# Kernel optimization log

Measured on AMD Instinct MI355X. Metric: run time of the kernel, lower is better.

Reference implementation:

```python
import jax, jax.numpy as jnp
import numpy as np

BEV_H = 128; BEV_W = 128; HEADS = 8; POINTS = 4; NUM_LAYERS = 6
PC = (-51.2, -51.2, -5.0, 51.2, 51.2, 3.0)
EPS = 1e-5


def _layernorm(x, g, b):
    m = x.mean(-1, keepdims=True)
    v = x.var(-1, keepdims=True)
    return (x - m) * jax.lax.rsqrt(v + 1e-5) * g + b


def _bilinear(feat, loc):
    # feat: (H, W, D); loc: (..., 2) normalized xy in [0, 1]; zero padding outside.
    H, W = feat.shape[0], feat.shape[1]
    ix = loc[..., 0] * W - 0.5
    iy = loc[..., 1] * H - 0.5
    x0 = jnp.floor(ix); y0 = jnp.floor(iy)
    fx = ix - x0; fy = iy - y0
    out = 0.0
    for dx in (0, 1):
        for dy in (0, 1):
            xi = x0 + dx; yi = y0 + dy
            w = (fx if dx else 1.0 - fx) * (fy if dy else 1.0 - fy)
            m = (xi >= 0) & (xi < W) & (yi >= 0) & (yi < H)
            xi_c = jnp.clip(xi, 0, W - 1).astype(jnp.int32)
            yi_c = jnp.clip(yi, 0, H - 1).astype(jnp.int32)
            out = out + (w * m)[..., None] * feat[yi_c, xi_c]
    return out


def _deform_grid(q, value, H, W, ref, ow, ob, aw, ab):
    # Deformable attention over a (H, W) grid of values; q: (Nq, C), value: (H*W, C).
    Nq, C = q.shape
    hd = C // HEADS
    v = value.reshape(H, W, HEADS, hd).transpose(2, 0, 1, 3)            # (h, H, W, hd)
    off = (q @ ow + ob).reshape(Nq, HEADS, POINTS, 2)
    loc = ref[:, None, None, :] + off / jnp.array([W, H], q.dtype)      # (Nq, h, P, 2)
    attn = jax.nn.softmax((q @ aw + ab).reshape(Nq, HEADS, POINTS), axis=-1)
    sampled = jax.vmap(_bilinear)(v, loc.transpose(1, 0, 2, 3))         # (h, Nq, P, hd)
    return jnp.einsum('hnpd,nhp->nhd', sampled, attn).reshape(Nq, C)


def _sca(q, feats, ref_cam, valid, ow, ob, aw, ab):
    # Spatial cross-attention: feats (Ncam, h, Hf, Wf, hd), ref_cam (Ncam, Nq, P, 2),
    # valid (Ncam, Nq, P) float mask of in-frustum projections.
    Nq, C = q.shape
    Hf, Wf = feats.shape[2], feats.shape[3]
    off = (q @ ow + ob).reshape(Nq, HEADS, POINTS, 2)
    loc = ref_cam[:, None] + (off / jnp.array([Wf, Hf], q.dtype)).transpose(1, 0, 2, 3)[None]
    # loc: (Ncam, h, Nq, P, 2)
    attn = jax.nn.softmax((q @ aw + ab).reshape(Nq, HEADS, POINTS), axis=-1)
    sampled = jax.vmap(jax.vmap(_bilinear))(feats, loc)                 # (Ncam, h, Nq, P, hd)
    num = jnp.einsum('chnpd,nhp,cnp->nhd', sampled, attn, valid)
    cnt = jnp.maximum(valid.sum((0, 2)), 1.0)                           # (Nq,)
    return (num / cnt[:, None, None]).reshape(Nq, C)


def _forward(image_feats, camera_intrinsics, camera_extrinsics, prev_bev, bev_embed,
             tsa_vw, tsa_vb, tsa_ow, tsa_ob, tsa_aw, tsa_ab, tsa_pw, tsa_pb,
             sca_vw, sca_vb, sca_ow, sca_ob, sca_aw, sca_ab, sca_pw, sca_pb,
             ffn_w1, ffn_b1, ffn_w2, ffn_b2,
             ln1_g, ln1_b, ln2_g, ln2_b, ln3_g, ln3_b):
    Ncam, C, Hf, Wf = image_feats.shape
    hd = C // HEADS
    Nq = BEV_H * BEV_W
    dt = image_feats.dtype
    feats_flat = image_feats.transpose(0, 2, 3, 1).reshape(Ncam * Hf * Wf, C)

    # 2D reference points for temporal self-attention (each query's own cell).
    xs = (jnp.arange(BEV_W, dtype=dt) + 0.5) / BEV_W
    ys = (jnp.arange(BEV_H, dtype=dt) + 0.5) / BEV_H
    gx, gy = jnp.meshgrid(xs, ys)                                       # (H, W) each
    ref2d = jnp.stack([gx.reshape(-1), gy.reshape(-1)], -1)             # (Nq, 2)

    # 3D pillar reference points projected into each camera.
    xm = PC[0] + gx.reshape(-1) * (PC[3] - PC[0])
    ym = PC[1] + gy.reshape(-1) * (PC[4] - PC[1])
    zm = PC[2] + (jnp.arange(POINTS, dtype=dt) + 0.5) / POINTS * (PC[5] - PC[2])
    ref3d = jnp.stack([
        jnp.broadcast_to(xm[:, None], (Nq, POINTS)),
        jnp.broadcast_to(ym[:, None], (Nq, POINTS)),
        jnp.broadcast_to(zm[None, :], (Nq, POINTS)),
        jnp.ones((Nq, POINTS), dt)], -1)                                # (Nq, P, 4)
    ego2cam = jnp.linalg.inv(camera_extrinsics[0])                      # (Ncam, 4, 4)
    pcam = jnp.einsum('cij,npj->cnpi', ego2cam, ref3d)[..., :3]
    img = jnp.einsum('cij,cnpj->cnpi', camera_intrinsics[0], pcam)
    z = img[..., 2]
    un = img[..., 0] / (jnp.maximum(z, EPS) * Wf)
    vn = img[..., 1] / (jnp.maximum(z, EPS) * Hf)
    valid = ((z > EPS) & (un >= 0) & (un <= 1) & (vn >= 0) & (vn <= 1)).astype(dt)
    ref_cam = jnp.stack([un, vn], -1)                                   # (Ncam, Nq, P, 2)

    q = bev_embed                                                       # (Nq, C)
    prev = prev_bev[:, 0, :]                                            # (Nq, C), B = 1
    for l in range(NUM_LAYERS):
        # Temporal self-attention: deformable sampling from prev BEV + current BEV.
        v_prev = prev @ tsa_vw[l] + tsa_vb[l]
        v_cur = q @ tsa_vw[l] + tsa_vb[l]
        a = 0.5 * (_deform_grid(q, v_prev, BEV_H, BEV_W, ref2d, tsa_ow[l], tsa_ob[l], tsa_aw[l], tsa_ab[l])
                   + _deform_grid(q, v_cur, BEV_H, BEV_W, ref2d, tsa_ow[l], tsa_ob[l], tsa_aw[l], tsa_ab[l]))
        q = _layernorm(q + a @ tsa_pw[l] + tsa_pb[l], ln1_g[l], ln1_b[l])
        # Spatial cross-attention over multi-camera image features.
        v_img = (feats_flat @ sca_vw[l] + sca_vb[l]).reshape(Ncam, Hf, Wf, HEADS, hd).transpose(0, 3, 1, 2, 4)
        a = _sca(q, v_img, ref_cam, valid, sca_ow[l], sca_ob[l], sca_aw[l], sca_ab[l])
        q = _layernorm(q + a @ sca_pw[l] + sca_pb[l], ln2_g[l], ln2_b[l])
        # FFN
        a = jax.nn.relu(q @ ffn_w1[l] + ffn_b1[l]) @ ffn_w2[l] + ffn_b2[l]
        q = _layernorm(q + a, ln3_g[l], ln3_b[l])
    return q.T.reshape(1, C, BEV_H, BEV_W)


def setup_inputs() -> dict:
    key = jax.random.key(0)
    ks = iter(jax.random.split(key, 80))
    def nrm(shape, s=0.02):
        return jax.random.normal(next(ks), shape, jnp.float32) * s
    C, L, Ncam, Hf, Wf = 256, NUM_LAYERS, 6, 58, 100
    Nq = BEV_H * BEV_W
    HP, HP2 = HEADS * POINTS, HEADS * POINTS * 2
    # Structured nuScenes-like cameras: 6 yaws at 60 deg, intrinsics at feature-map scale.
    extr = np.zeros((1, Ncam, 4, 4), np.float32)
    for c in range(Ncam):
        t = c * np.pi / 3.0
        f = np.array([np.cos(t), np.sin(t), 0.0])
        xc = np.array([np.sin(t), -np.cos(t), 0.0])
        yc = np.array([0.0, 0.0, -1.0])
        extr[0, c, :3, :3] = np.stack([xc, yc, f], axis=1)
        extr[0, c, :3, 3] = 1.5 * f + np.array([0.0, 0.0, 1.5])
        extr[0, c, 3, 3] = 1.0
    intr = np.zeros((1, Ncam, 3, 3), np.float32)
    intr[0, :, 0, 0] = 80.0; intr[0, :, 1, 1] = 80.0
    intr[0, :, 0, 2] = Wf / 2.0; intr[0, :, 1, 2] = Hf / 2.0
    intr[0, :, 2, 2] = 1.0
    return {
        'image_feats': jax.random.normal(next(ks), (Ncam, C, Hf, Wf), jnp.float32),
        'camera_intrinsics': jnp.asarray(intr),
        'camera_extrinsics': jnp.asarray(extr),
        'prev_bev': jax.random.normal(next(ks), (Nq, 1, C), jnp.float32),
        'bev_embed': nrm((Nq, C)),
        'tsa_vw': nrm((L, C, C)), 'tsa_vb': jnp.zeros((L, C), jnp.float32),
        'tsa_ow': nrm((L, C, HP2)), 'tsa_ob': nrm((L, HP2), 2.0),
        'tsa_aw': nrm((L, C, HP)), 'tsa_ab': jnp.zeros((L, HP), jnp.float32),
        'tsa_pw': nrm((L, C, C)), 'tsa_pb': jnp.zeros((L, C), jnp.float32),
        'sca_vw': nrm((L, C, C)), 'sca_vb': jnp.zeros((L, C), jnp.float32),
        'sca_ow': nrm((L, C, HP2)), 'sca_ob': nrm((L, HP2), 2.0),
        'sca_aw': nrm((L, C, HP)), 'sca_ab': jnp.zeros((L, HP), jnp.float32),
        'sca_pw': nrm((L, C, C)), 'sca_pb': jnp.zeros((L, C), jnp.float32),
        'ffn_w1': nrm((L, C, 2 * C)), 'ffn_b1': jnp.zeros((L, 2 * C), jnp.float32),
        'ffn_w2': nrm((L, 2 * C, C)), 'ffn_b2': jnp.zeros((L, C), jnp.float32),
        'ln1_g': jnp.ones((L, C), jnp.float32), 'ln1_b': jnp.zeros((L, C), jnp.float32),
        'ln2_g': jnp.ones((L, C), jnp.float32), 'ln2_b': jnp.zeros((L, C), jnp.float32),
        'ln3_g': jnp.ones((L, C), jnp.float32), 'ln3_b': jnp.zeros((L, C), jnp.float32),
    }


def reference(image_feats, camera_intrinsics, camera_extrinsics, prev_bev, bev_embed,
              tsa_vw, tsa_vb, tsa_ow, tsa_ob, tsa_aw, tsa_ab, tsa_pw, tsa_pb,
              sca_vw, sca_vb, sca_ow, sca_ob, sca_aw, sca_ab, sca_pw, sca_pb,
              ffn_w1, ffn_b1, ffn_w2, ffn_b2,
              ln1_g, ln1_b, ln2_g, ln2_b, ln3_g, ln3_b):
    return _forward(image_feats, camera_intrinsics, camera_extrinsics, prev_bev, bev_embed,
                    tsa_vw, tsa_vb, tsa_ow, tsa_ob, tsa_aw, tsa_ab, tsa_pw, tsa_pb,
                    sca_vw, sca_vb, sca_ow, sca_ob, sca_aw, sca_ab, sca_pw, sca_pb,
                    ffn_w1, ffn_b1, ffn_w2, ffn_b2,
                    ln1_g, ln1_b, ln2_g, ln2_b, ln3_g, ln3_b)
```

## Files before the change

kernel.cpp:

```cpp
#include <hip/hip_runtime.h>
#include <hip/hip_bf16.h>
#include <math.h>

typedef __hip_bfloat16 bf16;

#define NQ      16384
#define CDIM    256
#define NHEADS  8
#define NPOINTS 4
#define NCAM    6
#define HF      58
#define WF      100
#define HWF     (HF*WF)
#define NFEAT   (NCAM*HWF)
#define HD      32
#define NLAYERS 6

typedef __attribute__((ext_vector_type(8))) short short8;
typedef __attribute__((ext_vector_type(4))) float floatx4;

__device__ __forceinline__ float toF(float x) { return x; }
__device__ __forceinline__ float toF(bf16 x) { return __bfloat162float(x); }
__device__ __forceinline__ void storeD(float* p, float v) { *p = v; }
__device__ __forceinline__ void storeD(bf16* p, float v) { *p = __float2bfloat16(v); }

__device__ __forceinline__ float bfLo(unsigned u) { return __uint_as_float(u << 16); }
__device__ __forceinline__ float bfHi(unsigned u) { return __uint_as_float(u & 0xffff0000u); }

__device__ __forceinline__ void gload_lds16(const bf16* g, bf16* l) {
    __builtin_amdgcn_global_load_lds(
        (const __attribute__((address_space(1))) void*)(g),
        (__attribute__((address_space(3))) void*)(l), 16, 0, 0);
}

template <typename DT, bool RELU, bool STAGE>
__global__ __launch_bounds__(256) void gemm_mfma(
    const bf16* __restrict__ A, const bf16* __restrict__ BT,
    const float* __restrict__ bias, DT* __restrict__ D,
    int M, int N, int K, size_t sB, size_t sBias, size_t sD)
{
    int z = blockIdx.z;
    BT += (size_t)z * sB;
    bias += (size_t)z * sBias;
    D += (size_t)z * sD;

    __shared__ bf16 smem[STAGE ? 128 * 136 : 128 * 64];
    bf16* As = smem;
    bf16* Bs = smem + 128 * 32;

    int tid = threadIdx.x;
    int lane = tid & 63, w = tid >> 6;
    int wm = w & 1, wn = w >> 1;
    int l15 = lane & 15, quad = lane >> 4;
    int bm = blockIdx.y * 128, bn = blockIdx.x * 128;

    floatx4 acc[4][4];
#pragma unroll
    for (int i = 0; i < 4; i++)
#pragma unroll
        for (int j = 0; j < 4; j++)
            acc[i][j] = (floatx4){0.f, 0.f, 0.f, 0.f};

    int rsub = lane >> 2;
    int kc   = (lane & 3) * 8;

    for (int k0 = 0; k0 < K; k0 += 32) {
#pragma unroll
        for (int h = 0; h < 2; h++) {
            int r0 = w * 32 + h * 16;
            int gm = bm + r0 + rsub;
            if (gm > M - 1) gm = M - 1;
            gload_lds16(A + (size_t)gm * K + k0 + kc, &As[r0 * 32]);
            gload_lds16(BT + (size_t)(bn + r0 + rsub) * K + k0 + kc, &Bs[r0 * 32]);
        }
        __syncthreads();

        short8 a[4], b[4];
#pragma unroll
        for (int i = 0; i < 4; i++)
            a[i] = *(const short8*)(&As[(wm * 64 + i * 16 + l15) * 32 + quad * 8]);
#pragma unroll
        for (int j = 0; j < 4; j++)
            b[j] = *(const short8*)(&Bs[(wn * 64 + j * 16 + l15) * 32 + quad * 8]);
#pragma unroll
        for (int i = 0; i < 4; i++)
#pragma unroll
            for (int j = 0; j < 4; j++)
                acc[i][j] = __builtin_amdgcn_mfma_f32_16x16x32_bf16(
                    a[i], b[j], acc[i][j], 0, 0, 0);
        __syncthreads();
    }

    if (STAGE) {
#pragma unroll
        for (int i = 0; i < 4; i++) {
#pragma unroll
            for (int j = 0; j < 4; j++) {
                int col = wn * 64 + j * 16 + l15;
                float bv = bias[bn + col];
#pragma unroll
                for (int r = 0; r < 4; r++) {
                    int row = wm * 64 + i * 16 + quad * 4 + r;
                    float v = acc[i][j][r] + bv;
                    if (RELU) v = fmaxf(v, 0.f);
                    smem[row * 136 + col] = __float2bfloat16(v);
                }
            }
        }
        __syncthreads();
        int lr0 = tid >> 4;
        int ck  = tid & 15;
#pragma unroll
        for (int pass = 0; pass < 8; pass++) {
            int lr = pass * 16 + lr0;
            int gm = bm + lr;
            if (gm < M) {
                uint4 v = *(const uint4*)(&smem[lr * 136 + ck * 8]);
                *(uint4*)((bf16*)D + (size_t)gm * N + bn + ck * 8) = v;
            }
        }
    } else {
#pragma unroll
        for (int i = 0; i < 4; i++) {
#pragma unroll
            for (int j = 0; j < 4; j++) {
                int col = bn + wn * 64 + j * 16 + l15;
                float bv = bias[col];
#pragma unroll
                for (int r = 0; r < 4; r++) {
                    int row = bm + wm * 64 + i * 16 + quad * 4 + r;
                    if (row < M) {
                        float v = acc[i][j][r] + bv;
                        if (RELU) v = fmaxf(v, 0.f);
                        storeD(&D[(size_t)row * N + col], v);
                    }
                }
            }
        }
    }
}

__global__ __launch_bounds__(256) void gemm_tsa(
    const bf16* __restrict__ A, const bf16* __restrict__ BT,
    const float* __restrict__ bias,
    bf16* __restrict__ vgrid, float* __restrict__ offlog)
{
    int bn3 = blockIdx.x;
    int bm = blockIdx.y * 128;
    if (bn3 == 2 && bm < NQ) return;
    int bn = bn3 * 128;

    __shared__ bf16 As[128 * 32];
    __shared__ bf16 Bs[128 * 32];

    int tid = threadIdx.x;
    int lane = tid & 63, w = tid >> 6;
    int wm = w & 1, wn = w >> 1;
    int l15 = lane & 15, quad = lane >> 4;

    floatx4 acc[4][4];
#pragma unroll
    for (int i = 0; i < 4; i++)
#pragma unroll
        for (int j = 0; j < 4; j++)
            acc[i][j] = (floatx4){0.f, 0.f, 0.f, 0.f};

    int rsub = lane >> 2;
    int kc   = (lane & 3) * 8;

    for (int k0 = 0; k0 < 256; k0 += 32) {
#pragma unroll
        for (int h = 0; h < 2; h++) {
            int r0 = w * 32 + h * 16;
            gload_lds16(A + (size_t)(bm + r0 + rsub) * 256 + k0 + kc, &As[r0 * 32]);
            gload_lds16(BT + (size_t)(bn + r0 + rsub) * 256 + k0 + kc, &Bs[r0 * 32]);
        }
        __syncthreads();

        short8 a[4], b[4];
#pragma unroll
        for (int i = 0; i < 4; i++)
            a[i] = *(const short8*)(&As[(wm * 64 + i * 16 + l15) * 32 + quad * 8]);
#pragma unroll
        for (int j = 0; j < 4; j++)
            b[j] = *(const short8*)(&Bs[(wn * 64 + j * 16 + l15) * 32 + quad * 8]);
#pragma unroll
        for (int i = 0; i < 4; i++)
#pragma unroll
            for (int j = 0; j < 4; j++)
                acc[i][j] = __builtin_amdgcn_mfma_f32_16x16x32_bf16(
                    a[i], b[j], acc[i][j], 0, 0, 0);
        __syncthreads();
    }

#pragma unroll
    for (int i = 0; i < 4; i++) {
#pragma unroll
        for (int j = 0; j < 4; j++) {
            int col = bn + wn * 64 + j * 16 + l15;
            float bv = bias[col];
#pragma unroll
            for (int r = 0; r < 4; r++) {
                int row = bm + wm * 64 + i * 16 + quad * 4 + r;
                float v = acc[i][j][r] + bv;
                if (bn3 < 2) {
                    int n = row & (NQ - 1);
                    int cur = row >= NQ;
                    size_t idx = ((size_t)n * 64 + (col >> 2)) * 8 + cur * 4 + (col & 3);
                    vgrid[idx] = __float2bfloat16(v);
                } else {
                    offlog[(size_t)(row - NQ) * 128 + (col - 256)] = v;
                }
            }
        }
    }
}

__global__ __launch_bounds__(512) void gemm_ln(
    const bf16* __restrict__ A, const bf16* __restrict__ BT,
    const float* __restrict__ bias,
    bf16* __restrict__ qb,
    const float* __restrict__ g, const float* __restrict__ b,
    int K)
{
    __shared__ bf16 As[64 * 32];
    __shared__ bf16 Bs[256 * 32];
    __shared__ float red[2][64][4];
    __shared__ float stats[2][64];

    int tid = threadIdx.x;
    int lane = tid & 63, w = tid >> 6;
    int wm = w & 1, wn = w >> 1;
    int l15 = lane & 15, quad = lane >> 4;
    int bm = blockIdx.x * 64;

    floatx4 acc[2][4];
#pragma unroll
    for (int i = 0; i < 2; i++)
#pragma unroll
        for (int j = 0; j < 4; j++)
            acc[i][j] = (floatx4){0.f, 0.f, 0.f, 0.f};

    int rsub = lane >> 2;
    int kc   = (lane & 3) * 8;

    for (int k0 = 0; k0 < K; k0 += 32) {
#pragma unroll
        for (int h = 0; h < 2; h++) {
            int r0 = w * 32 + h * 16;
            gload_lds16(BT + (size_t)(r0 + rsub) * K + k0 + kc, &Bs[r0 * 32]);
        }
        if (w < 4)
            gload_lds16(A + (size_t)(bm + w * 16 + rsub) * K + k0 + kc,
                        &As[w * 16 * 32]);
        __syncthreads();

        short8 a[2], bfr[4];
#pragma unroll
        for (int i = 0; i < 2; i++)
            a[i] = *(const short8*)(&As[(wm * 32 + i * 16 + l15) * 32 + quad * 8]);
#pragma unroll
        for (int j = 0; j < 4; j++)
            bfr[j] = *(const short8*)(&Bs[(wn * 64 + j * 16 + l15) * 32 + quad * 8]);
#pragma unroll
        for (int i = 0; i < 2; i++)
#pragma unroll
            for (int j = 0; j < 4; j++)
                acc[i][j] = __builtin_amdgcn_mfma_f32_16x16x32_bf16(
                    a[i], bfr[j], acc[i][j], 0, 0, 0);
        __syncthreads();
    }

    float x[2][4][4];
#pragma unroll
    for (int i = 0; i < 2; i++) {
#pragma unroll
        for (int j = 0; j < 4; j++) {
            int col = wn * 64 + j * 16 + l15;
            float bv = bias[col];
#pragma unroll
            for (int r = 0; r < 4; r++) {
                int row = bm + wm * 32 + i * 16 + quad * 4 + r;
                x[i][j][r] = toF(qb[(size_t)row * CDIM + col]) + acc[i][j][r] + bv;
            }
        }
    }
#pragma unroll
    for (int i = 0; i < 2; i++) {
#pragma unroll
        for (int r = 0; r < 4; r++) {
            float s = x[i][0][r] + x[i][1][r] + x[i][2][r] + x[i][3][r];
            float sq = x[i][0][r] * x[i][0][r] + x[i][1][r] * x[i][1][r] +
                       x[i][2][r] * x[i][2][r] + x[i][3][r] * x[i][3][r];
#pragma unroll
            for (int m = 1; m < 16; m <<= 1) {
                s += __shfl_xor(s, m);
                sq += __shfl_xor(sq, m);
            }
            if (l15 == 0) {
                int rl = wm * 32 + i * 16 + quad * 4 + r;
                red[0][rl][wn] = s;
                red[1][rl][wn] = sq;
            }
        }
    }
    __syncthreads();
    if (tid < 64) {
        float s = red[0][tid][0] + red[0][tid][1] + red[0][tid][2] + red[0][tid][3];
        float sq = red[1][tid][0] + red[1][tid][1] + red[1][tid][2] + red[1][tid][3];
        float mean = s * (1.f / CDIM);
        float var = fmaxf(sq * (1.f / CDIM) - mean * mean, 0.f);
        stats[0][tid] = mean;
        stats[1][tid] = rsqrtf(var + 1e-5f);
    }
    __syncthreads();
#pragma unroll
    for (int i = 0; i < 2; i++) {
#pragma unroll
        for (int j = 0; j < 4; j++) {
            int col = wn * 64 + j * 16 + l15;
            float gc = g[col], bc = b[col];
#pragma unroll
            for (int r = 0; r < 4; r++) {
                int rl = wm * 32 + i * 16 + quad * 4 + r;
                int row = bm + rl;
                float y = (x[i][j][r] - stats[0][rl]) * stats[1][rl] * gc + bc;
                qb[(size_t)row * CDIM + col] = __float2bfloat16(y);
            }
        }
    }
}

__global__ void wt_cvt_kernel(const float* __restrict__ W, bf16* __restrict__ WT,
                              int K, int N)
{
    __shared__ float tile[32][33];
    int l = blockIdx.z;
    const float* Wl = W + (size_t)l * K * N;
    bf16* WTl = WT + (size_t)l * K * N;
    int k0 = blockIdx.x * 32, n0 = blockIdx.y * 32;
    int tx = threadIdx.x, ty = threadIdx.y;
    for (int i = 0; i < 32; i += 8)
        tile[ty + i][tx] = Wl[(size_t)(k0 + ty + i) * N + n0 + tx];
    __syncthreads();
    for (int i = 0; i < 32; i += 8)
        WTl[(size_t)(n0 + ty + i) * K + k0 + tx] = __float2bfloat16(tile[tx][ty + i]);
}

__global__ void pack_tsa_kernel(const float* __restrict__ vw, const float* __restrict__ vb,
                                const float* __restrict__ ow, const float* __restrict__ ob,
                                const float* __restrict__ aw, const float* __restrict__ ab,
                                bf16* __restrict__ WT, float* __restrict__ BIAS)
{
    int n = blockIdx.x;
    int l = blockIdx.y;
    int k = threadIdx.x;
    float v = 0.f;
    if (n < 256)      v = vw[((size_t)l * 256 + k) * 256 + n];
    else if (n < 320) v = ow[((size_t)l * 256 + k) * 64 + (n - 256)];
    else if (n < 352) v = aw[((size_t)l * 256 + k) * 32 + (n - 320)];
    WT[((size_t)l * 384 + n) * 256 + k] = __float2bfloat16(v);
    if (k == 0) {
        float bv = 0.f;
        if (n < 256)      bv = vb[l * 256 + n];
        else if (n < 320) bv = ob[l * 64 + (n - 256)];
        else if (n < 352) bv = ab[l * 32 + (n - 320)];
        BIAS[l * 384 + n] = bv;
    }
}

__global__ void pack_offattn_kernel(const float* __restrict__ ow, const float* __restrict__ ob,
                                    const float* __restrict__ aw, const float* __restrict__ ab,
                                    bf16* __restrict__ WT, float* __restrict__ BIAS)
{
    int l = blockIdx.y;
    int n = blockIdx.x;
    int k = threadIdx.x;
    float v = 0.f;
    if (n < 64)      v = ow[((size_t)l * 256 + k) * 64 + n];
    else if (n < 96) v = aw[((size_t)l * 256 + k) * 32 + (n - 64)];
    WT[((size_t)l * 128 + n) * 256 + k] = __float2bfloat16(v);
    if (k == 0) {
        float bv = 0.f;
        if (n < 64)      bv = ob[l * 64 + n];
        else if (n < 96) bv = ab[l * 32 + (n - 64)];
        BIAS[l * 128 + n] = bv;
    }
}

__global__ void feats_cvt_kernel(const float* __restrict__ in, bf16* __restrict__ outT)
{
    __shared__ float tile[32][33];
    int c = blockIdx.z;
    int r0 = blockIdx.x * 32, ch0 = blockIdx.y * 32;
    int tx = threadIdx.x, ty = threadIdx.y;
    for (int i = 0; i < 32; i += 8) {
        int r = r0 + tx, ch = ch0 + ty + i;
        tile[ty + i][tx] = (r < HWF) ? in[((size_t)c * CDIM + ch) * HWF + r] : 0.f;
    }
    __syncthreads();
    for (int i = 0; i < 32; i += 8) {
        int r = r0 + ty + i, ch = ch0 + tx;
        if (r < HWF)
            outT[((size_t)c * HWF + r) * CDIM + ch] = __float2bfloat16(tile[tx][ty + i]);
    }
}

__global__ __launch_bounds__(256) void cvt_bf16_kernel(const float* __restrict__ in,
                                                       bf16* __restrict__ out, int n)
{
    int i = blockIdx.x * 256 + threadIdx.x;
    if (i < n) out[i] = __float2bfloat16(in[i]);
}

__global__ void invert4_kernel(const float* __restrict__ extr, float* __restrict__ ego)
{
    int c = threadIdx.x;
    if (c >= NCAM) return;
    float a[4][8];
    for (int i = 0; i < 4; i++)
        for (int j = 0; j < 4; j++) {
            a[i][j] = extr[c * 16 + i * 4 + j];
            a[i][4 + j] = (i == j) ? 1.f : 0.f;
        }
    for (int col = 0; col < 4; col++) {
        int piv = col;
        float best = fabsf(a[col][col]);
        for (int r = col + 1; r < 4; r++) {
            float v = fabsf(a[r][col]);
            if (v > best) { best = v; piv = r; }
        }
        if (piv != col)
            for (int j = 0; j < 8; j++) {
                float t = a[col][j]; a[col][j] = a[piv][j]; a[piv][j] = t;
            }
        float inv = 1.f / a[col][col];
        for (int j = 0; j < 8; j++) a[col][j] *= inv;
        for (int r = 0; r < 4; r++) {
            if (r == col) continue;
            float f = a[r][col];
            for (int j = 0; j < 8; j++) a[r][j] -= f * a[col][j];
        }
    }
    for (int i = 0; i < 4; i++)
        for (int j = 0; j < 4; j++)
            ego[c * 16 + i * 4 + j] = a[i][4 + j];
}

__global__ __launch_bounds__(256) void refcam_kernel(
    const float* __restrict__ ego, const float* __restrict__ intr,
    float* __restrict__ refcam, float* __restrict__ validb)
{
    int t = blockIdx.x * 256 + threadIdx.x;
    if (t >= NCAM * NQ * NPOINTS) return;
    int p = t & 3;
    int n = (t >> 2) & (NQ - 1);
    int c = t >> 16;

    float gx = ((n & 127) + 0.5f) / 128.0f;
    float gy = ((n >> 7) + 0.5f) / 128.0f;
    float xm = -51.2f + gx * 102.4f;
    float ym = -51.2f + gy * 102.4f;
    float zm = -5.0f + (p + 0.5f) * 2.0f;

    const float* E = ego + c * 16;
    float pc[3];
#pragma unroll
    for (int i = 0; i < 3; i++)
        pc[i] = E[i * 4 + 0] * xm + E[i * 4 + 1] * ym + E[i * 4 + 2] * zm + E[i * 4 + 3];

    const float* I = intr + c * 9;
    float im[3];
#pragma unroll
    for (int i = 0; i < 3; i++)
        im[i] = I[i * 3 + 0] * pc[0] + I[i * 3 + 1] * pc[1] + I[i * 3 + 2] * pc[2];

    float z = im[2];
    float zc = fmaxf(z, 1e-5f);
    float un = im[0] / (zc * (float)WF);
    float vn = im[1] / (zc * (float)HF);
    float val = (z > 1e-5f && un >= 0.f && un <= 1.f && vn >= 0.f && vn <= 1.f) ? 1.f : 0.f;

    size_t idx = ((size_t)c * NQ + n) * NPOINTS + p;
    refcam[idx * 2] = un;
    refcam[idx * 2 + 1] = vn;
    validb[idx] = val;
}

__global__ __launch_bounds__(256) void tsa_sample_kernel(
    const bf16* __restrict__ vgrid, const float* __restrict__ offlog,
    bf16* __restrict__ outA)
{
    int blk = blockIdx.x;
    int qq = (blk & 7) * 512 + (blk >> 3);
    int t = threadIdx.x;
    int n = qq * 4 + (t >> 6);
    int r = t & 63;
    int h = r >> 3;
    int dq = r & 7;
    int col = h * HD + dq * 4;
    int q8 = h * 8 + dq;

    const float* fl = offlog + (size_t)n * 128;
    const float* lg = fl + 64 + h * 4;
    float l0 = lg[0], l1 = lg[1], l2 = lg[2], l3 = lg[3];
    float mx = fmaxf(fmaxf(l0, l1), fmaxf(l2, l3));
    float e0 = expf(l0 - mx), e1 = expf(l1 - mx), e2 = expf(l2 - mx), e3 = expf(l3 - mx);
    float inv = 1.f / (e0 + e1 + e2 + e3);
    float w[4] = { e0 * inv, e1 * inv, e2 * inv, e3 * inv };

    const float* of = fl + h * 8;
    float rx = ((n & 127) + 0.5f) / 128.f;
    float ry = ((n >> 7) + 0.5f) / 128.f;

    float a0 = 0.f, a1 = 0.f, a2 = 0.f, a3 = 0.f;
#pragma unroll
    for (int p = 0; p < NPOINTS; p++) {
        float lx = rx + of[p * 2] * (1.f / 128.f);
        float ly = ry + of[p * 2 + 1] * (1.f / 128.f);
        float ix = lx * 128.f - 0.5f;
        float iy = ly * 128.f - 0.5f;
        float xf = floorf(ix), yf = floorf(iy);
        float fx = ix - xf, fy = iy - yf;
        int x0 = (int)xf, y0 = (int)yf;
#pragma unroll
        for (int dy = 0; dy < 2; dy++) {
            int yi = y0 + dy;
            if (yi < 0 || yi >= 128) continue;
            float wy = dy ? fy : 1.f - fy;
#pragma unroll
            for (int dx = 0; dx < 2; dx++) {
                int xi = x0 + dx;
                if (xi < 0 || xi >= 128) continue;
                float wgt = w[p] * wy * (dx ? fx : 1.f - fx);
                size_t idx = ((size_t)(yi * 128 + xi) * 64 + q8) * 8;
                uint4 v = *(const uint4*)(vgrid + idx);
                a0 += wgt * (bfLo(v.x) + bfLo(v.z));
                a1 += wgt * (bfHi(v.x) + bfHi(v.z));
                a2 += wgt * (bfLo(v.y) + bfLo(v.w));
                a3 += wgt * (bfHi(v.y) + bfHi(v.w));
            }
        }
    }
    union { bf16 b[4]; uint2 u; } pk;
    pk.b[0] = __float2bfloat16(0.5f * a0);
    pk.b[1] = __float2bfloat16(0.5f * a1);
    pk.b[2] = __float2bfloat16(0.5f * a2);
    pk.b[3] = __float2bfloat16(0.5f * a3);
    *(uint2*)(outA + (size_t)n * CDIM + col) = pk.u;
}

__global__ __launch_bounds__(256) void sca_sample_kernel(
    const bf16* __restrict__ vimg, const float* __restrict__ offlog,
    const float* __restrict__ refcam, const float* __restrict__ validb,
    bf16* __restrict__ outA)
{
    int blk = blockIdx.x;
    int qo = (blk & 7) * 256 + (blk >> 3);
    int t = threadIdx.x;
    int n = qo * 8 + (t >> 5);
    int r = t & 31;
    int h = r >> 2;
    int d8 = r & 3;
    int col = h * HD + d8 * 8;

    const float* fl = offlog + (size_t)n * 128;
    const float* lg = fl + 64 + h * 4;
    float l0 = lg[0], l1 = lg[1], l2 = lg[2], l3 = lg[3];
    float mx = fmaxf(fmaxf(l0, l1), fmaxf(l2, l3));
    float e0 = expf(l0 - mx), e1 = expf(l1 - mx), e2 = expf(l2 - mx), e3 = expf(l3 - mx);
    float inv = 1.f / (e0 + e1 + e2 + e3);
    float w[4] = { e0 * inv, e1 * inv, e2 * inv, e3 * inv };

    const float* of = fl + h * 8;
    float ox[4], oy[4];
#pragma unroll
    for (int p = 0; p < NPOINTS; p++) {
        ox[p] = of[p * 2] * (1.f / (float)WF);
        oy[p] = of[p * 2 + 1] * (1.f / (float)HF);
    }

    float a0 = 0.f, a1 = 0.f, a2 = 0.f, a3 = 0.f;
    float a4 = 0.f, a5 = 0.f, a6 = 0.f, a7 = 0.f;
    float vsum = 0.f;
    for (int c = 0; c < NCAM; c++) {
        const bf16* vb = vimg + (size_t)c * HWF * CDIM;
        size_t base = ((size_t)c * NQ + n) * NPOINTS;
#pragma unroll
        for (int p = 0; p < NPOINTS; p++) {
            float vl = validb[base + p];
            vsum += vl;
            if (vl == 0.f) continue;
            float lx = refcam[(base + p) * 2] + ox[p];
            float ly = refcam[(base + p) * 2 + 1] + oy[p];
            float ix = lx * (float)WF - 0.5f;
            float iy = ly * (float)HF - 0.5f;
            float xf = floorf(ix), yf = floorf(iy);
            float fx = ix - xf, fy = iy - yf;
            int x0 = (int)xf, y0 = (int)yf;
            float wp_ = w[p] * vl;
#pragma unroll
            for (int dy = 0; dy < 2; dy++) {
                int yi = y0 + dy;
                if (yi < 0 || yi >= HF) continue;
                float wy = dy ? fy : 1.f - fy;
#pragma unroll
                for (int dx = 0; dx < 2; dx++) {
                    int xi = x0 + dx;
                    if (xi < 0 || xi >= WF) continue;
                    float wgt = wp_ * wy * (dx ? fx : 1.f - fx);
                    uint4 u = *(const uint4*)(vb + (size_t)(yi * WF + xi) * CDIM + col);
                    a0 += wgt * bfLo(u.x);
                    a1 += wgt * bfHi(u.x);
                    a2 += wgt * bfLo(u.y);
                    a3 += wgt * bfHi(u.y);
                    a4 += wgt * bfLo(u.z);
                    a5 += wgt * bfHi(u.z);
                    a6 += wgt * bfLo(u.w);
                    a7 += wgt * bfHi(u.w);
                }
            }
        }
    }
    float ic = 1.f / fmaxf(vsum, 1.f);
    union { bf16 b[8]; uint4 u; } pk;
    pk.b[0] = __float2bfloat16(a0 * ic);
    pk.b[1] = __float2bfloat16(a1 * ic);
    pk.b[2] = __float2bfloat16(a2 * ic);
    pk.b[3] = __float2bfloat16(a3 * ic);
    pk.b[4] = __float2bfloat16(a4 * ic);
    pk.b[5] = __float2bfloat16(a5 * ic);
    pk.b[6] = __float2bfloat16(a6 * ic);
    pk.b[7] = __float2bfloat16(a7 * ic);
    *(uint4*)(outA + (size_t)n * CDIM + col) = pk.u;
}

__global__ void out_transpose_kernel(const bf16* __restrict__ qb, float* __restrict__ out)
{
    __shared__ float tile[32][33];
    int n0 = blockIdx.x * 32;
    int c0 = blockIdx.y * 32;
    int tx = threadIdx.x, ty = threadIdx.y;
    for (int i = 0; i < 32; i += 8)
        tile[ty + i][tx] = toF(qb[(size_t)(n0 + ty + i) * CDIM + c0 + tx]);
    __syncthreads();
    for (int i = 0; i < 32; i += 8)
        out[(size_t)(c0 + ty + i) * NQ + n0 + tx] = tile[tx][ty + i];
}

extern "C" void kernel_launch(void* const* d_in, const int* in_sizes, int n_in,
                              void* d_out, int out_size, void* d_ws, size_t ws_size,
                              hipStream_t stream)
{
    const float* image_feats = (const float*)d_in[0];
    const float* intr        = (const float*)d_in[1];
    const float* extr        = (const float*)d_in[2];
    const float* prev_bev    = (const float*)d_in[3];
    const float* bev_embed   = (const float*)d_in[4];
    const float* tsa_vw = (const float*)d_in[5];
    const float* tsa_vb = (const float*)d_in[6];
    const float* tsa_ow = (const float*)d_in[7];
    const float* tsa_ob = (const float*)d_in[8];
    const float* tsa_aw = (const float*)d_in[9];
    const float* tsa_ab = (const float*)d_in[10];
    const float* tsa_pw = (const float*)d_in[11];
    const float* tsa_pb = (const float*)d_in[12];
    const float* sca_vw = (const float*)d_in[13];
    const float* sca_vb = (const float*)d_in[14];
    const float* sca_ow = (const float*)d_in[15];
    const float* sca_ob = (const float*)d_in[16];
    const float* sca_aw = (const float*)d_in[17];
    const float* sca_ab = (const float*)d_in[18];
    const float* sca_pw = (const float*)d_in[19];
    const float* sca_pb = (const float*)d_in[20];
    const float* ffn_w1 = (const float*)d_in[21];
    const float* ffn_b1 = (const float*)d_in[22];
    const float* ffn_w2 = (const float*)d_in[23];
    const float* ffn_b2 = (const float*)d_in[24];
    const float* ln1_g  = (const float*)d_in[25];
    const float* ln1_b  = (const float*)d_in[26];
    const float* ln2_g  = (const float*)d_in[27];
    const float* ln2_b  = (const float*)d_in[28];
    const float* ln3_g  = (const float*)d_in[29];
    const float* ln3_b  = (const float*)d_in[30];

    char* wp = (char*)d_ws;
    auto alloc = [&](size_t bytes) -> void* {
        void* r = (void*)wp;
        wp += (bytes + 255) & ~(size_t)255;
        return r;
    };
    bf16*  prevbf = (bf16*) alloc((size_t)NQ * CDIM * 2);
    bf16*  qb     = (bf16*) alloc((size_t)NQ * CDIM * 2);
    bf16*  attnA  = (bf16*) alloc((size_t)NQ * CDIM * 2);
    float* offlog = (float*)alloc((size_t)NQ * 128 * 4);
    float* refcam = (float*)alloc((size_t)NCAM * NQ * NPOINTS * 2 * 4);
    float* validb = (float*)alloc((size_t)NCAM * NQ * NPOINTS * 4);
    float* ego    = (float*)alloc(128 * 4);
    bf16*  featsT = (bf16*) alloc((size_t)NFEAT * CDIM * 2);
    bf16*  pwT  = (bf16*)alloc((size_t)NLAYERS * 65536 * 2);
    bf16*  svwT = (bf16*)alloc((size_t)NLAYERS * 65536 * 2);
    bf16*  spwT = (bf16*)alloc((size_t)NLAYERS * 65536 * 2);
    bf16*  w1T  = (bf16*)alloc((size_t)NLAYERS * 131072 * 2);
    bf16*  w2T  = (bf16*)alloc((size_t)NLAYERS * 131072 * 2);
    bf16*  ptwT = (bf16*)alloc((size_t)NLAYERS * 384 * 256 * 2);
    float* ptb  = (float*)alloc((size_t)NLAYERS * 384 * 4);
    bf16*  sowT = (bf16*)alloc((size_t)NLAYERS * 32768 * 2);
    float* sobF = (float*)alloc((size_t)NLAYERS * 128 * 4);
    bf16*  vgrid = (bf16*)alloc((size_t)NQ * CDIM * 2 * 2);
    bf16*  vimg6 = (bf16*)alloc((size_t)NLAYERS * NFEAT * CDIM * 2);

    bf16* hidden = featsT;

    dim3 blk32(32, 8);

    cvt_bf16_kernel<<<(NQ * CDIM + 255) / 256, 256, 0, stream>>>(bev_embed, qb, NQ * CDIM);
    cvt_bf16_kernel<<<(NQ * CDIM + 255) / 256, 256, 0, stream>>>(prev_bev, prevbf, NQ * CDIM);
    invert4_kernel<<<1, 64, 0, stream>>>(extr, ego);
    refcam_kernel<<<(NCAM * NQ * NPOINTS + 255) / 256, 256, 0, stream>>>(ego, intr, refcam, validb);
    {
        dim3 g((HWF + 31) / 32, CDIM / 32, NCAM);
        feats_cvt_kernel<<<g, blk32, 0, stream>>>(image_feats, featsT);
    }
    wt_cvt_kernel<<<dim3(8, 8,  NLAYERS), blk32, 0, stream>>>(tsa_pw, pwT,  256, 256);
    wt_cvt_kernel<<<dim3(8, 8,  NLAYERS), blk32, 0, stream>>>(sca_vw, svwT, 256, 256);
    wt_cvt_kernel<<<dim3(8, 8,  NLAYERS), blk32, 0, stream>>>(sca_pw, spwT, 256, 256);
    wt_cvt_kernel<<<dim3(8, 16, NLAYERS), blk32, 0, stream>>>(ffn_w1, w1T, 256, 512);
    wt_cvt_kernel<<<dim3(16, 8, NLAYERS), blk32, 0, stream>>>(ffn_w2, w2T, 512, 256);
    pack_tsa_kernel<<<dim3(384, NLAYERS), 256, 0, stream>>>(
        tsa_vw, tsa_vb, tsa_ow, tsa_ob, tsa_aw, tsa_ab, ptwT, ptb);
    pack_offattn_kernel<<<dim3(128, NLAYERS), 256, 0, stream>>>(
        sca_ow, sca_ob, sca_aw, sca_ab, sowT, sobF);
    gemm_mfma<bf16, false, true><<<dim3(2, (NFEAT + 127) / 128, NLAYERS), 256, 0, stream>>>(
        featsT, svwT, sca_vb, vimg6, NFEAT, CDIM, CDIM,
        65536, 256, (size_t)NFEAT * CDIM);

    for (int l = 0; l < NLAYERS; l++) {
        gemm_tsa<<<dim3(3, 2 * NQ / 128), 256, 0, stream>>>(
            prevbf, ptwT + (size_t)l * 98304, ptb + l * 384, vgrid, offlog);
        tsa_sample_kernel<<<NQ / 4, 256, 0, stream>>>(vgrid, offlog, attnA);
        gemm_ln<<<NQ / 64, 512, 0, stream>>>(
            attnA, pwT + (size_t)l * 65536, tsa_pb + l * CDIM,
            qb, ln1_g + l * CDIM, ln1_b + l * CDIM, CDIM);

        gemm_mfma<float, false, false><<<dim3(1, NQ / 128, 1), 256, 0, stream>>>(
            qb, sowT + (size_t)l * 32768, sobF + l * 128, offlog, NQ, 128, CDIM, 0, 0, 0);
        sca_sample_kernel<<<NQ / 8, 256, 0, stream>>>(
            vimg6 + (size_t)l * NFEAT * CDIM, offlog, refcam, validb, attnA);
        gemm_ln<<<NQ / 64, 512, 0, stream>>>(
            attnA, spwT + (size_t)l * 65536, sca_pb + l * CDIM,
            qb, ln2_g + l * CDIM, ln2_b + l * CDIM, CDIM);

        gemm_mfma<bf16, true, true><<<dim3(4, NQ / 128, 1), 256, 0, stream>>>(
            qb, w1T + (size_t)l * 131072, ffn_b1 + l * 512, hidden, NQ, 512, CDIM, 0, 0, 0);
        gemm_ln<<<NQ / 64, 512, 0, stream>>>(
            hidden, w2T + (size_t)l * 131072, ffn_b2 + l * CDIM,
            qb, ln3_g + l * CDIM, ln3_b + l * CDIM, 512);
    }

    {
        dim3 g(NQ / 32, CDIM / 32);
        out_transpose_kernel<<<g, blk32, 0, stream>>>(qb, (float*)d_out);
    }
}
```

Baseline: 1.069 ms.

## Swizzle LDS layouts in MFMA GEMMs and add A-resident multi-layer image value GEMM

Applies an XOR swizzle to the LDS chunk layout in all MFMA GEMM kernels so that short8 fragment reads avoid LDS bank conflicts. Replaces the per-layer image value projection launch with a new kernel that loads a 64-row A tile (full K=256) into LDS once and reuses it across all six layers' weights. The B tiles are double-buffered, and output is staged through LDS for coalesced 16-byte stores. This cuts repeated global reads of the image features, at the cost of larger LDS use per block and fewer, longer-running blocks.

Measured after the change: 1.071 ms. About the same (+0.2%).

```diff
diff --git a/kernel.cpp b/kernel.cpp
--- a/kernel.cpp
+++ b/kernel.cpp
@@ -33,6 +33,7 @@
         (__attribute__((address_space(3))) void*)(l), 16, 0, 0);
 }
 
+
 template <typename DT, bool RELU, bool STAGE>
 __global__ __launch_bounds__(256) void gemm_mfma(
     const bf16* __restrict__ A, const bf16* __restrict__ BT,
@@ -62,7 +63,8 @@
             acc[i][j] = (floatx4){0.f, 0.f, 0.f, 0.f};
 
     int rsub = lane >> 2;
-    int kc   = (lane & 3) * 8;
+    int kc   = (((lane & 3) ^ ((rsub >> 1) & 3))) * 8;
+    int sw   = (l15 >> 1) & 3;
 
     for (int k0 = 0; k0 < K; k0 += 32) {
 #pragma unroll
@@ -78,10 +80,10 @@
         short8 a[4], b[4];
 #pragma unroll
         for (int i = 0; i < 4; i++)
-            a[i] = *(const short8*)(&As[(wm * 64 + i * 16 + l15) * 32 + quad * 8]);
+            a[i] = *(const short8*)(&As[(wm * 64 + i * 16 + l15) * 32 + (quad ^ sw) * 8]);
 #pragma unroll
         for (int j = 0; j < 4; j++)
-            b[j] = *(const short8*)(&Bs[(wn * 64 + j * 16 + l15) * 32 + quad * 8]);
+            b[j] = *(const short8*)(&Bs[(wn * 64 + j * 16 + l15) * 32 + (quad ^ sw) * 8]);
 #pragma unroll
         for (int i = 0; i < 4; i++)
 #pragma unroll
@@ -140,6 +142,113 @@
     }
 }
 
+__global__ __launch_bounds__(256) void gemm_vimg(
+    const bf16* __restrict__ A,
+    const bf16* __restrict__ BT,
+    const float* __restrict__ bias,
+    bf16* __restrict__ D)
+{
+    __shared__ bf16 As[64 * 256];
+    __shared__ bf16 Bs[2][256 * 32];
+    __shared__ bf16 Cs[16 * 264];
+
+    int tid = threadIdx.x;
+    int lane = tid & 63, w = tid >> 6;
+    int l15 = lane & 15, quad = lane >> 4;
+    int bm = blockIdx.x * 64;
+
+    {
+        int rs2 = lane >> 5;
+        int ch  = lane & 31;
+#pragma unroll
+        for (int h = 0; h < 8; h++) {
+            int rloc = w * 16 + h * 2 + rs2;
+            int gm = bm + rloc;
+            if (gm > NFEAT - 1) gm = NFEAT - 1;
+            int sc = (ch ^ (rloc & 7)) * 8;
+            gload_lds16(A + (size_t)gm * 256 + sc, &As[(w * 16 + h * 2) * 256]);
+        }
+    }
+
+    int rsub = lane >> 2;
+    int bchunk = ((lane & 3) ^ ((rsub >> 1) & 3)) * 8;
+    auto stageB = [&](int buf, int z, int kk) {
+        const bf16* src = BT + (size_t)z * 65536 + kk * 32;
+#pragma unroll
+        for (int h2 = 0; h2 < 4; h2++) {
+            int r0 = w * 64 + h2 * 16;
+            gload_lds16(src + (size_t)(r0 + rsub) * 256 + bchunk, &Bs[buf][r0 * 32]);
+        }
+    };
+
+    stageB(0, 0, 0);
+    __syncthreads();
+
+    int sA = l15 & 7;
+    int sB = (l15 >> 1) & 3;
+
+    for (int z = 0; z < 6; z++) {
+        floatx4 acc[4][4];
+#pragma unroll
+        for (int i = 0; i < 4; i++)
+#pragma unroll
+            for (int j = 0; j < 4; j++)
+                acc[i][j] = (floatx4){0.f, 0.f, 0.f, 0.f};
+
+        for (int kk = 0; kk < 8; kk++) {
+            int t = z * 8 + kk;
+            int cur = t & 1;
+            if (t + 1 < 48)
+                stageB(cur ^ 1, (t + 1) >> 3, (t + 1) & 7);
+
+            short8 a[4], b[4];
+#pragma unroll
+            for (int i = 0; i < 4; i++)
+                a[i] = *(const short8*)(
+                    &As[(i * 16 + l15) * 256 + (((kk * 4 + quad) ^ sA) * 8)]);
+#pragma unroll
+            for (int j = 0; j < 4; j++)
+                b[j] = *(const short8*)(
+                    &Bs[cur][(w * 64 + j * 16 + l15) * 32 + ((quad ^ sB) * 8)]);
+#pragma unroll
+            for (int i = 0; i < 4; i++)
+#pragma unroll
+                for (int j = 0; j < 4; j++)
+                    acc[i][j] = __builtin_amdgcn_mfma_f32_16x16x32_bf16(
+                        a[i], b[j], acc[i][j], 0, 0, 0);
+
+            if (kk == 7) {
+                const float* bz = bias + z * 256;
+                bf16* Dz = D + (size_t)z * NFEAT * 256;
+#pragma unroll
+                for (int q2 = 0; q2 < 4; q2++) {
+                    __syncthreads();
+#pragma unroll
+                    for (int j = 0; j < 4; j++) {
+                        int col = w * 64 + j * 16 + l15;
+                        float bv = bz[col];
+#pragma unroll
+                        for (int r = 0; r < 4; r++)
+                            Cs[(quad * 4 + r) * 264 + col] =
+                                __float2bfloat16(acc[q2][j][r] + bv);
+                    }
+                    __syncthreads();
+#pragma unroll
+                    for (int s2 = 0; s2 < 2; s2++) {
+                        int rl = s2 * 8 + (tid >> 5);
+                        int gm = bm + q2 * 16 + rl;
+                        if (gm < NFEAT) {
+                            uint4 v = *(const uint4*)(&Cs[rl * 264 + (tid & 31) * 8]);
+                            *(uint4*)(Dz + (size_t)gm * 256 + (tid & 31) * 8) = v;
+                        }
+                    }
+                }
+            }
+            __syncthreads();
+        }
+    }
+}
+
 __global__ __launch_bounds__(256) void gemm_tsa(
     const bf16* __restrict__ A, const bf16* __restrict__ BT,
     const float* __restrict__ bias,
@@ -166,7 +275,8 @@
             acc[i][j] = (floatx4){0.f, 0.f, 0.f, 0.f};
 
     int rsub = lane >> 2;
-    int kc   = (lane & 3) * 8;
+    int kc   = (((lane & 3) ^ ((rsub >> 1) & 3))) * 8;
+    int sw   = (l15 >> 1) & 3;
 
     for (int k0 = 0; k0 < 256; k0 += 32) {
 #pragma unroll
@@ -180,10 +290,10 @@
         short8 a[4], b[4];
 #pragma unroll
         for (int i = 0; i < 4; i++)
-            a[i] = *(const short8*)(&As[(wm * 64 + i * 16 + l15) * 32 + quad * 8]);
+            a[i] = *(const short8*)(&As[(wm * 64 + i * 16 + l15) * 32 + (quad ^ sw) * 8]);
 #pragma unroll
         for (int j = 0; j < 4; j++)
-            b[j] = *(const short8*)(&Bs[(wn * 64 + j * 16 + l15) * 32 + quad * 8]);
+            b[j] = *(const short8*)(&Bs[(wn * 64 + j * 16 + l15) * 32 + (quad ^ sw) * 8]);
 #pragma unroll
         for (int i = 0; i < 4; i++)
 #pragma unroll
@@ -242,7 +352,8 @@
             acc[i][j] = (floatx4){0.f, 0.f, 0.f, 0.f};
 
     int rsub = lane >> 2;
-    int kc   = (lane & 3) * 8;
+    int kc   = (((lane & 3) ^ ((rsub >> 1) & 3))) * 8;
+    int sw   = (l15 >> 1) & 3;
 
     for (int k0 = 0; k0 < K; k0 += 32) {
 #pragma unroll
@@ -258,10 +369,10 @@
         short8 a[2], bfr[4];
 #pragma unroll
         for (int i = 0; i < 2; i++)
-            a[i] = *(const short8*)(&As[(wm * 32 + i * 16 + l15) * 32 + quad * 8]);
+            a[i] = *(const short8*)(&As[(wm * 32 + i * 16 + l15) * 32 + (quad ^ sw) * 8]);
 #pragma unroll
         for (int j = 0; j < 4; j++)
-            bfr[j] = *(const short8*)(&Bs[(wn * 64 + j * 16 + l15) * 32 + quad * 8]);
+            bfr[j] = *(const short8*)(&Bs[(wn * 64 + j * 16 + l15) * 32 + (quad ^ sw) * 8]);
 #pragma unroll
         for (int i = 0; i < 2; i++)
 #pragma unroll
@@ -731,9 +842,7 @@
         tsa_vw, tsa_vb, tsa_ow, tsa_ob, tsa_aw, tsa_ab, ptwT, ptb);
     pack_offattn_kernel<<<dim3(128, NLAYERS), 256, 0, stream>>>(
         sca_ow, sca_ob, sca_aw, sca_ab, sowT, sobF);
-    gemm_mfma<bf16, false, true><<<dim3(2, (NFEAT + 127) / 128, NLAYERS), 256, 0, stream>>>(
-        featsT, svwT, sca_vb, vimg6, NFEAT, CDIM, CDIM,
-        65536, 256, (size_t)NFEAT * CDIM);
+    gemm_vimg<<<dim3((NFEAT + 63) / 64), 256, 0, stream>>>(featsT, svwT, sca_vb, vimg6);
 
     for (int l = 0; l < NLAYERS; l++) {
         gemm_tsa<<<dim3(3, 2 * NQ / 128), 256, 0, stream>>>(
```

## Swizzle LDS tiles in MFMA GEMMs, add small-tile offset GEMM, reorder layer grid

Applied to the files above, without the earlier changes.

XOR-swizzles the 16-byte chunk index used when writing and reading the A/B LDS tiles in all MFMA GEMMs, to reduce LDS bank conflicts on the fragment reads. Adds a dedicated 64x64-tile GEMM for the N=128 offset/attention projection so that launch uses more, smaller blocks instead of 128 large ones. The batched image-value GEMM now folds the layer index into blockIdx.x, so blocks for all layers that share the same A rows run close together and can reuse them in cache. The swizzle has to match between the global-to-LDS load and the fragment reads, and the smaller tiles give less reuse per block.

Measured after the change: 993.3 us. 7.1% less time.

```diff
diff --git a/kernel.cpp b/kernel.cpp
--- a/kernel.cpp
+++ b/kernel.cpp
@@ -33,13 +33,21 @@
         (__attribute__((address_space(3))) void*)(l), 16, 0, 0);
 }
 
-template <typename DT, bool RELU, bool STAGE>
+
+template <typename DT, bool RELU, bool STAGE, bool ZF>
 __global__ __launch_bounds__(256) void gemm_mfma(
     const bf16* __restrict__ A, const bf16* __restrict__ BT,
     const float* __restrict__ bias, DT* __restrict__ D,
     int M, int N, int K, size_t sB, size_t sBias, size_t sD)
 {
-    int z = blockIdx.z;
+    int z, bn;
+    if (ZF) {
+        z  = blockIdx.x % NLAYERS;
+        bn = (blockIdx.x / NLAYERS) * 128;
+    } else {
+        z  = blockIdx.z;
+        bn = blockIdx.x * 128;
+    }
     BT += (size_t)z * sB;
     bias += (size_t)z * sBias;
     D += (size_t)z * sD;
@@ -52,7 +60,7 @@
     int lane = tid & 63, w = tid >> 6;
     int wm = w & 1, wn = w >> 1;
     int l15 = lane & 15, quad = lane >> 4;
-    int bm = blockIdx.y * 128, bn = blockIdx.x * 128;
+    int bm = blockIdx.y * 128;
 
     floatx4 acc[4][4];
 #pragma unroll
@@ -62,7 +70,8 @@
             acc[i][j] = (floatx4){0.f, 0.f, 0.f, 0.f};
 
     int rsub = lane >> 2;
-    int kc   = (lane & 3) * 8;
+    int kc   = (((lane & 3) ^ ((rsub >> 1) & 3))) * 8;
+    int sw   = (l15 >> 1) & 3;
 
     for (int k0 = 0; k0 < K; k0 += 32) {
 #pragma unroll
@@ -78,10 +87,10 @@
         short8 a[4], b[4];
 #pragma unroll
         for (int i = 0; i < 4; i++)
-            a[i] = *(const short8*)(&As[(wm * 64 + i * 16 + l15) * 32 + quad * 8]);
+            a[i] = *(const short8*)(&As[(wm * 64 + i * 16 + l15) * 32 + (quad ^ sw) * 8]);
 #pragma unroll
         for (int j = 0; j < 4; j++)
-            b[j] = *(const short8*)(&Bs[(wn * 64 + j * 16 + l15) * 32 + quad * 8]);
+            b[j] = *(const short8*)(&Bs[(wn * 64 + j * 16 + l15) * 32 + (quad ^ sw) * 8]);
 #pragma unroll
         for (int i = 0; i < 4; i++)
 #pragma unroll
@@ -140,6 +149,55 @@
     }
 }
 
+__global__ __launch_bounds__(256) void gemm_off(
+    const bf16* __restrict__ A, const bf16* __restrict__ BT,
+    const float* __restrict__ bias, float* __restrict__ D)
+{
+    __shared__ bf16 As[64 * 32];
+    __shared__ bf16 Bs[64 * 32];
+
+    int tid = threadIdx.x;
+    int lane = tid & 63, w = tid >> 6;
+    int l15 = lane & 15, quad = lane >> 4;
+    int bm = blockIdx.y * 64, bn = blockIdx.x * 64;
+
+    floatx4 acc[4];
+#pragma unroll
+    for (int j = 0; j < 4; j++)
+        acc[j] = (floatx4){0.f, 0.f, 0.f, 0.f};
+
+    int rsub = lane >> 2;
+    int kc   = (((lane & 3) ^ ((rsub >> 1) & 3))) * 8;
+    int sw   = (l15 >> 1) & 3;
+
+    for (int k0 = 0; k0 < 256; k0 += 32) {
+        gload_lds16(A + (size_t)(bm + w * 16 + rsub) * 256 + k0 + kc, &As[w * 16 * 32]);
+        gload_lds16(BT + (size_t)(bn + w * 16 + rsub) * 256 + k0 + kc, &Bs[w * 16 * 32]);
+        __syncthreads();
+
+        short8 a = *(const short8*)(&As[(w * 16 + l15) * 32 + (quad ^ sw) * 8]);
+        short8 b[4];
+#pragma unroll
+        for (int j = 0; j < 4; j++)
+            b[j] = *(const short8*)(&Bs[(j * 16 + l15) * 32 + (quad ^ sw) * 8]);
+#pragma unroll
+        for (int j = 0; j < 4; j++)
+            acc[j] = __builtin_amdgcn_mfma_f32_16x16x32_bf16(a, b[j], acc[j], 0, 0, 0);
+        __syncthreads();
+    }
+
+#pragma unroll
+    for (int j = 0; j < 4; j++) {
+        int col = bn + j * 16 + l15;
+        float bv = bias[col];
+#pragma unroll
+        for (int r = 0; r < 4; r++) {
+            int row = bm + w * 16 + quad * 4 + r;
+            D[(size_t)row * 128 + col] = acc[j][r] + bv;
+        }
+    }
+}
+
 __global__ __launch_bounds__(256) void gemm_tsa(
     const bf16* __restrict__ A, const bf16* __restrict__ BT,
     const float* __restrict__ bias,
@@ -166,7 +224,8 @@
             acc[i][j] = (floatx4){0.f, 0.f, 0.f, 0.f};
 
     int rsub = lane >> 2;
-    int kc   = (lane & 3) * 8;
+    int kc   = (((lane & 3) ^ ((rsub >> 1) & 3))) * 8;
+    int sw   = (l15 >> 1) & 3;
 
     for (int k0 = 0; k0 < 256; k0 += 32) {
 #pragma unroll
@@ -180,10 +239,10 @@
         short8 a[4], b[4];
 #pragma unroll
         for (int i = 0; i < 4; i++)
-            a[i] = *(const short8*)(&As[(wm * 64 + i * 16 + l15) * 32 + quad * 8]);
+            a[i] = *(const short8*)(&As[(wm * 64 + i * 16 + l15) * 32 + (quad ^ sw) * 8]);
 #pragma unroll
         for (int j = 0; j < 4; j++)
-            b[j] = *(const short8*)(&Bs[(wn * 64 + j * 16 + l15) * 32 + quad * 8]);
+            b[j] = *(const short8*)(&Bs[(wn * 64 + j * 16 + l15) * 32 + (quad ^ sw) * 8]);
 #pragma unroll
         for (int i = 0; i < 4; i++)
 #pragma unroll
@@ -242,7 +301,8 @@
             acc[i][j] = (floatx4){0.f, 0.f, 0.f, 0.f};
 
     int rsub = lane >> 2;
-    int kc   = (lane & 3) * 8;
+    int kc   = (((lane & 3) ^ ((rsub >> 1) & 3))) * 8;
+    int sw   = (l15 >> 1) & 3;
 
     for (int k0 = 0; k0 < K; k0 += 32) {
 #pragma unroll
@@ -258,10 +318,10 @@
         short8 a[2], bfr[4];
 #pragma unroll
         for (int i = 0; i < 2; i++)
-            a[i] = *(const short8*)(&As[(wm * 32 + i * 16 + l15) * 32 + quad * 8]);
+            a[i] = *(const short8*)(&As[(wm * 32 + i * 16 + l15) * 32 + (quad ^ sw) * 8]);
 #pragma unroll
         for (int j = 0; j < 4; j++)
-            bfr[j] = *(const short8*)(&Bs[(wn * 64 + j * 16 + l15) * 32 + quad * 8]);
+            bfr[j] = *(const short8*)(&Bs[(wn * 64 + j * 16 + l15) * 32 + (quad ^ sw) * 8]);
 #pragma unroll
         for (int i = 0; i < 2; i++)
 #pragma unroll
@@ -731,7 +791,7 @@
         tsa_vw, tsa_vb, tsa_ow, tsa_ob, tsa_aw, tsa_ab, ptwT, ptb);
     pack_offattn_kernel<<<dim3(128, NLAYERS), 256, 0, stream>>>(
         sca_ow, sca_ob, sca_aw, sca_ab, sowT, sobF);
-    gemm_mfma<bf16, false, true><<<dim3(2, (NFEAT + 127) / 128, NLAYERS), 256, 0, stream>>>(
+    gemm_mfma<bf16, false, true, true><<<dim3(2 * NLAYERS, (NFEAT + 127) / 128, 1), 256, 0, stream>>>(
         featsT, svwT, sca_vb, vimg6, NFEAT, CDIM, CDIM,
         65536, 256, (size_t)NFEAT * CDIM);
 
@@ -743,15 +803,15 @@
             attnA, pwT + (size_t)l * 65536, tsa_pb + l * CDIM,
             qb, ln1_g + l * CDIM, ln1_b + l * CDIM, CDIM);
 
-        gemm_mfma<float, false, false><<<dim3(1, NQ / 128, 1), 256, 0, stream>>>(
-            qb, sowT + (size_t)l * 32768, sobF + l * 128, offlog, NQ, 128, CDIM, 0, 0, 0);
+        gemm_off<<<dim3(2, NQ / 64), 256, 0, stream>>>(
+            qb, sowT + (size_t)l * 32768, sobF + l * 128, offlog);
         sca_sample_kernel<<<NQ / 8, 256, 0, stream>>>(
             vimg6 + (size_t)l * NFEAT * CDIM, offlog, refcam, validb, attnA);
         gemm_ln<<<NQ / 64, 512, 0, stream>>>(
             attnA, spwT + (size_t)l * 65536, sca_pb + l * CDIM,
             qb, ln2_g + l * CDIM, ln2_b + l * CDIM, CDIM);
 
-        gemm_mfma<bf16, true, true><<<dim3(4, NQ / 128, 1), 256, 0, stream>>>(
+        gemm_mfma<bf16, true, true, false><<<dim3(4, NQ / 128, 1), 256, 0, stream>>>(
             qb, w1T + (size_t)l * 131072, ffn_b1 + l * 512, hidden, NQ, 512, CDIM, 0, 0, 0);
         gemm_ln<<<NQ / 64, 512, 0, stream>>>(
             hidden, w2T + (size_t)l * 131072, ffn_b2 + l * CDIM,
```
